# Optimization experiments

Measured on AMD Instinct MI355X. Metric: run time of the kernel, lower is better.

## Reference

```python
import jax, jax.numpy as jnp
import numpy as np

N = 8192
IN_F = 300
OUT_F = 300
ALPHA = 0.3  # leaky relu slope
NEG_INF = -1e12


def setup_inputs() -> dict:
    key = jax.random.key(0)
    k1, k2, k3, k4, k5 = jax.random.split(key, 5)
    inp = jax.random.normal(k1, (N, IN_F), dtype=jnp.float32)
    adj = jax.random.randint(k2, (N, N), 0, 2, dtype=jnp.int32)
    # xavier-uniform-like init for params
    def xavier(k, shape):
        fan_in, fan_out = shape[0], shape[1]
        limit = 1.414 * (6.0 / (fan_in + fan_out)) ** 0.5
        return jax.random.uniform(k, shape, jnp.float32, -limit, limit)
    W = xavier(k3, (IN_F, OUT_F))
    a = xavier(k4, (2 * OUT_F, 1))
    wtrans = xavier(k5, (2 * IN_F, OUT_F))
    return {"inp": inp, "adj": adj, "W": W, "a": a, "wtrans": wtrans}


def reference(inp, adj, W, a, wtrans):
    # h: [N, OUT_F]
    h = inp @ W
    Wh1 = h @ a[:OUT_F, :]          # [N, 1]
    Wh2 = h @ a[OUT_F:, :]          # [N, 1]
    e = jax.nn.leaky_relu(Wh1 + Wh2.T, negative_slope=ALPHA)  # [N, N]
    mask = adj > 0
    attention = jax.nn.softmax(jnp.where(mask, e, NEG_INF), axis=1)
    negative_attention = -jax.nn.softmax(jnp.where(mask, -e, NEG_INF), axis=1)
    # dropout p=0.0 / eval mode -> identity
    h_prime = attention @ inp                 # [N, IN_F]
    h_prime_negative = negative_attention @ inp
    h_prime_double = jnp.concatenate([h_prime, h_prime_negative], axis=1)  # [N, 2*IN_F]
    new_h_prime = h_prime_double @ wtrans     # [N, OUT_F]
    return jax.nn.elu(new_h_prime)  # concat=True
```

## Files before the change

kernel.cpp:

```cpp
#include <hip/hip_runtime.h>
#include <stdint.h>

#define NROW 8192
#define LOG2E 1.4426950408889634f
#define ALPHA 0.3f

#define WA1_OFF 0
#define WA2_OFF 512
#define S1_OFF 1024
#define S2_OFF (1024 + 8192)
#define SCAL_OFF (S2_OFF + 8192)
#define PQB_OFF 70656
#define PQB_BYTES (256 * 40960)
#define AMSK_OFF (PQB_OFF + PQB_BYTES)
#define AMSK_BYTES (NROW * 256 * 4)
#define PART_OFF (AMSK_OFF + AMSK_BYTES)

typedef _Float16 f16x8 __attribute__((ext_vector_type(8)));
typedef __fp16 fp16x2 __attribute__((ext_vector_type(2)));
typedef float f32x4 __attribute__((ext_vector_type(4)));

union HPack { fp16x2 h2[4]; f16x8 v; uint32_t u[4]; };
union HBits { _Float16 h[2]; uint32_t u; };

__device__ __forceinline__ int swz(int col, int g) { return (g + (col >> 1)) & 3; }

__global__ void k_wa(const float* __restrict__ Wm, const float* __restrict__ a,
                     float* __restrict__ wsf) {
  int r = blockIdx.x * 4 + (threadIdx.x >> 6);
  int ln = threadIdx.x & 63;
  if (r >= 300) return;
  float a1 = 0.f, a2 = 0.f;
  for (int c = ln; c < 300; c += 64) {
    float w = Wm[r * 300 + c];
    a1 += w * a[c];
    a2 += w * a[300 + c];
  }
  for (int o = 32; o; o >>= 1) { a1 += __shfl_down(a1, o); a2 += __shfl_down(a2, o); }
  if (!ln) { wsf[WA1_OFF + r] = a1; wsf[WA2_OFF + r] = a2; }
}

__global__ void k_s12(const float* __restrict__ inp, float* __restrict__ wsf) {
  int row = blockIdx.x * 4 + (threadIdx.x >> 6);
  int ln = threadIdx.x & 63;
  const float* ip = inp + (size_t)row * 300;
  float a1 = 0.f, a2 = 0.f;
  for (int c = ln; c < 300; c += 64) {
    float v = ip[c];
    a1 += v * wsf[WA1_OFF + c];
    a2 += v * wsf[WA2_OFF + c];
  }
  for (int o = 32; o; o >>= 1) { a1 += __shfl_down(a1, o); a2 += __shfl_down(a2, o); }
  if (!ln) { wsf[S1_OFF + row] = a1 * LOG2E; wsf[S2_OFF + row] = a2 * LOG2E; }
}

__global__ void k_minmax(float* __restrict__ wsf) {
  int t = threadIdx.x;
  float mx = -3e38f, mn = 3e38f;
  for (int i = t; i < NROW; i += 1024) {
    float v = wsf[S2_OFF + i];
    mx = fmaxf(mx, v); mn = fminf(mn, v);
  }
  for (int o = 32; o; o >>= 1) {
    mx = fmaxf(mx, __shfl_down(mx, o));
    mn = fminf(mn, __shfl_down(mn, o));
  }
  __shared__ float sm[32];
  int wv = t >> 6, ln = t & 63;
  if (!ln) { sm[wv] = mx; sm[16 + wv] = mn; }
  __syncthreads();
  if (!t) {
    float M = sm[0], m = sm[16];
    for (int q = 1; q < 16; q++) { M = fmaxf(M, sm[q]); m = fminf(m, sm[16 + q]); }
    wsf[SCAL_OFF] = M; wsf[SCAL_OFF + 1] = m;
  }
}

__global__ __launch_bounds__(256) void k_pack(const int* __restrict__ adj,
                                              uint32_t* __restrict__ amask) {
  const size_t t = (size_t)blockIdx.x * 256 + threadIdx.x;
  const int4* src = (const int4*)(adj + t * 32);
  uint32_t m = 0;
  #pragma unroll
  for (int j = 0; j < 8; j++) {
    int4 v = src[j];
    m |= (v.x ? 1u : 0u) << (4 * j);
    m |= (v.y ? 1u : 0u) << (4 * j + 1);
    m |= (v.z ? 1u : 0u) << (4 * j + 2);
    m |= (v.w ? 1u : 0u) << (4 * j + 3);
  }
  amask[t] = m;
}

__global__ __launch_bounds__(640) void k_wt(const float* __restrict__ inp,
                                            const float* __restrict__ wt,
                                            uint16_t* __restrict__ pqb) {
  __shared__ float L[300 * 36];
  const int kb = blockIdx.x;
  const int t = threadIdx.x;
  const float* src = inp + (size_t)kb * 32 * 300;
  for (int idx = t; idx < 9600; idx += 640) {
    int j = idx / 300;
    int c = idx - j * 300;
    L[c * 36 + j] = src[idx];
  }
  __syncthreads();
  if (t < 608) {
    const int pq = (t >= 304) ? 1 : 0;
    const int f = t - pq * 304;
    float acc[32];
    if (f < 300) {
      #pragma unroll
      for (int q = 0; q < 32; q++) acc[q] = 0.f;
      const float* wcol = wt + (size_t)pq * 90000 + f;
      for (int c = 0; c < 300; c++) {
        float wv = wcol[(size_t)c * 300];
        const float4* lp = (const float4*)(L + c * 36);
        #pragma unroll
        for (int q = 0; q < 8; q++) {
          float4 v = lp[q];
          acc[q * 4 + 0] += v.x * wv;
          acc[q * 4 + 1] += v.y * wv;
          acc[q * 4 + 2] += v.z * wv;
          acc[q * 4 + 3] += v.w * wv;
        }
      }
    } else {
      float cv = (f == 300) ? 1.0f : 0.0f;
      #pragma unroll
      for (int q = 0; q < 32; q++) acc[q] = cv;
    }
    uint16_t* dst = pqb + (size_t)kb * 20480 + (size_t)pq * 10240 + (size_t)f * 32;
    #pragma unroll
    for (int g = 0; g < 4; g++) {
      const int gs = swz(f, g);
      uint32_t* d32 = (uint32_t*)(dst + gs * 8);
      #pragma unroll
      for (int i = 0; i < 4; i++) {
        HBits hb;
        hb.h[0] = (_Float16)acc[g * 8 + 2 * i];
        hb.h[1] = (_Float16)acc[g * 8 + 2 * i + 1];
        d32[i] = hb.u;
      }
    }
  }
}

__global__ __launch_bounds__(512, 2) void k_main(const uint32_t* __restrict__ amask,
                                                 const float* __restrict__ wsf,
                                                 const uint16_t* __restrict__ pqb,
                                                 float* __restrict__ part, int nsplit) {
  __shared__ __align__(16) uint16_t Bsm[3][20480];
  const int bid = blockIdx.x;
  const int mblk = bid / nsplit;
  const int ks = bid - mblk * nsplit;
  const int tid = threadIdx.x;
  const int w = tid >> 6, lane = tid & 63;
  const int lr = lane & 15, lg = lane >> 4;
  const int side = w & 1;
  const int rg = w >> 1;
  const int rbase = mblk * 128 + rg * 32;
  const int row0 = rbase + lr;
  const int row1 = rbase + 16 + lr;
  const float c1_0 = wsf[S1_OFF + row0];
  const float c1_1 = wsf[S1_OFF + row1];
  const float s2ref = side ? wsf[SCAL_OFF + 1] : wsf[SCAL_OFF];
  const float sgn = side ? -1.0f : 1.0f;
  float tt0 = c1_0 + s2ref; const float so0 = sgn * fmaxf(tt0, ALPHA * tt0);
  float tt1 = c1_1 + s2ref; const float so1 = sgn * fmaxf(tt1, ALPHA * tt1);
  const int kcnt = NROW / nsplit;
  const int k0 = ks * kcnt;
  const int ksteps = kcnt >> 5;
  const int tb0 = k0 >> 5;
  const uint32_t* mr0 = amask + (size_t)row0 * 256;
  const uint32_t* mr1 = amask + (size_t)row1 * 256;
  f32x4 acc0[19], acc1[19];
  const f32x4 zero = {0.f, 0.f, 0.f, 0.f};
  #pragma unroll
  for (int ct = 0; ct < 19; ct++) { acc0[ct] = zero; acc1[ct] = zero; }

  auto STAGE = [&](int b, int tb) {
    const char* tile = (const char*)(pqb + (size_t)tb * 20480);
    char* dst = (char*)Bsm[b];
    #pragma unroll
    for (int it = 0; it < 5; it++) {
      const int off = (w * 5 + it) * 1024;
      __builtin_amdgcn_global_load_lds(
          (const __attribute__((address_space(1))) void*)(tile + off + lane * 16),
          (__attribute__((address_space(3))) void*)(dst + off),
          16, 0, 0);
    }
  };

  STAGE(0, tb0);
  uint32_t cM0 = mr0[tb0];
  uint32_t cM1 = mr1[tb0];
  const int kw0 = k0 + lg * 8;
  float4 cS0 = *(const float4*)(wsf + S2_OFF + kw0);
  float4 cS1 = *(const float4*)(wsf + S2_OFF + kw0 + 4);
  STAGE(1, (ksteps > 1) ? tb0 + 1 : tb0);

  for (int s = 0; s < ksteps; s++) {
    const int cur = s % 3;
    const int sp = (s + 1 < ksteps) ? s + 1 : s;
    const uint32_t nM0 = mr0[tb0 + sp];
    const uint32_t nM1 = mr1[tb0 + sp];
    const int kwn = k0 + sp * 32 + lg * 8;
    const float4 nS0 = *(const float4*)(wsf + S2_OFF + kwn);
    const float4 nS1 = *(const float4*)(wsf + S2_OFF + kwn + 4);

    asm volatile("s_waitcnt vmcnt(9)" ::: "memory");
    __builtin_amdgcn_sched_barrier(0);
    __builtin_amdgcn_s_barrier();

    const int st = (s + 2 < ksteps) ? s + 2 : ksteps - 1;
    STAGE((s + 2) % 3, tb0 + st);

    float se[8] = {cS0.x, cS0.y, cS0.z, cS0.w, cS1.x, cS1.y, cS1.z, cS1.w};
    const uint32_t b0 = (cM0 >> (lg * 8)) & 0xffu;
    const uint32_t b1 = (cM1 >> (lg * 8)) & 0xffu;
    HPack up0, up1;
    #pragma unroll
    for (int e = 0; e < 8; e += 2) {
      float e0a = c1_0 + se[e];     e0a = fmaxf(e0a, ALPHA * e0a);
      float e0b = c1_0 + se[e + 1]; e0b = fmaxf(e0b, ALPHA * e0b);
      float e1a = c1_1 + se[e];     e1a = fmaxf(e1a, ALPHA * e1a);
      float e1b = c1_1 + se[e + 1]; e1b = fmaxf(e1b, ALPHA * e1b);
      float p0a = exp2f(__builtin_fmaf(sgn, e0a, -so0)); p0a = (b0 & (1u << e)) ? p0a : 0.0f;
      float p0b = exp2f(__builtin_fmaf(sgn, e0b, -so0)); p0b = (b0 & (2u << e)) ? p0b : 0.0f;
      float p1a = exp2f(__builtin_fmaf(sgn, e1a, -so1)); p1a = (b1 & (1u << e)) ? p1a : 0.0f;
      float p1b = exp2f(__builtin_fmaf(sgn, e1b, -so1)); p1b = (b1 & (2u << e)) ? p1b : 0.0f;
      up0.h2[e >> 1] = __builtin_amdgcn_cvt_pkrtz(p0a, p0b);
      up1.h2[e >> 1] = __builtin_amdgcn_cvt_pkrtz(p1a, p1b);
    }

    const char* half = (const char*)Bsm[cur] + side * 20480;
    #pragma unroll
    for (int ct = 0; ct < 19; ct++) {
      const int col = ct * 16 + lr;
      const int gp = swz(col, lg);
      f16x8 b = *(const f16x8*)(half + col * 64 + gp * 16);
      acc0[ct] = __builtin_amdgcn_mfma_f32_16x16x32_f16(up0.v, b, acc0[ct], 0, 0, 0);
      acc1[ct] = __builtin_amdgcn_mfma_f32_16x16x32_f16(up1.v, b, acc1[ct], 0, 0, 0);
    }

    cM0 = nM0; cM1 = nM1; cS0 = nS0; cS1 = nS1;
  }

  float* pb = part + ((size_t)ks * NROW + rbase) * 608 + (size_t)side * 304;
  #pragma unroll
  for (int ct = 0; ct < 19; ct++) {
    const int col = ct * 16 + lr;
    #pragma unroll
    for (int r = 0; r < 4; r++) {
      pb[(size_t)(lg * 4 + r) * 608 + col] = acc0[ct][r];
      pb[(size_t)(16 + lg * 4 + r) * 608 + col] = acc1[ct][r];
    }
  }
}

__global__ void k_final(const float* __restrict__ part, float* __restrict__ out, int nsplit) {
  const int i = blockIdx.x;
  const int t = threadIdx.x;
  if (t >= 300) return;
  float sp = 0.f, sn = 0.f, zp = 0.f, zn = 0.f;
  for (int s = 0; s < nsplit; s++) {
    const float* p = part + ((size_t)s * NROW + i) * 608;
    sp += p[t];
    sn += p[304 + t];
    zp += p[300];
    zn += p[604];
  }
  float x = sp / zp - sn / zn;
  out[(size_t)i * 300 + t] = (x > 0.f) ? x : (exp2f(x * LOG2E) - 1.0f);
}

extern "C" void kernel_launch(void* const* d_in, const int* in_sizes, int n_in,
                              void* d_out, int out_size, void* d_ws, size_t ws_size,
                              hipStream_t stream) {
  const float* inp = (const float*)d_in[0];
  const int* adj = (const int*)d_in[1];
  const float* Wm = (const float*)d_in[2];
  const float* a = (const float*)d_in[3];
  const float* wt = (const float*)d_in[4];
  float* out = (float*)d_out;
  float* wsf = (float*)d_ws;
  uint16_t* pqb = (uint16_t*)((char*)d_ws + PQB_OFF);
  uint32_t* amask = (uint32_t*)((char*)d_ws + AMSK_OFF);
  float* part = (float*)((char*)d_ws + PART_OFF);

  int nsplit = 4;
  while (nsplit > 1 &&
         (size_t)PART_OFF + (size_t)nsplit * NROW * 608 * 4 > ws_size)
    nsplit >>= 1;

  k_wa<<<75, 256, 0, stream>>>(Wm, a, wsf);
  k_s12<<<NROW / 4, 256, 0, stream>>>(inp, wsf);
  k_minmax<<<1, 1024, 0, stream>>>(wsf);
  k_pack<<<NROW * NROW / 32 / 256, 256, 0, stream>>>(adj, amask);
  k_wt<<<256, 640, 0, stream>>>(inp, wt, pqb);
  k_main<<<64 * nsplit, 512, 0, stream>>>(amask, wsf, pqb, part, nsplit);
  k_final<<<NROW, 320, 0, stream>>>(part, out, nsplit);
}
```

Measured before the change: 270.6 us.

## Compute inp·wtrans with MFMA and fuse it with adjacency bit-packing

The fp32 scalar inp·wtrans projection is replaced by an fp16 MFMA GEMM. Wtrans is pre-converted to a swizzled fp16 layout by a new small kernel and streamed into LDS via double-buffered global_load_lds. The adjacency mask packing runs as extra blocks of the same launch, so the bandwidth-bound pack can overlap the compute-bound projection. s_setprio is also raised around the MFMA loop in k_main. The fp16 rounding of inp and wtrans before accumulation adds some precision loss.

```diff
diff --git a/kernel.cpp b/kernel.cpp
--- a/kernel.cpp
+++ b/kernel.cpp
@@ -14,14 +14,16 @@
 #define PQB_BYTES (256 * 40960)
 #define AMSK_OFF (PQB_OFF + PQB_BYTES)
 #define AMSK_BYTES (NROW * 256 * 4)
-#define PART_OFF (AMSK_OFF + AMSK_BYTES)
+#define WTF_OFF (AMSK_OFF + AMSK_BYTES)
+#define WTF_BYTES (10 * 40960)
+#define PART_OFF (WTF_OFF + WTF_BYTES)
 
 typedef _Float16 f16x8 __attribute__((ext_vector_type(8)));
 typedef __fp16 fp16x2 __attribute__((ext_vector_type(2)));
 typedef float f32x4 __attribute__((ext_vector_type(4)));
 
 union HPack { fp16x2 h2[4]; f16x8 v; uint32_t u[4]; };
-union HBits { _Float16 h[2]; uint32_t u; };
+union PkU { fp16x2 p; uint32_t u; };
 
 __device__ __forceinline__ int swz(int col, int g) { return (g + (col >> 1)) & 3; }
 
@@ -76,72 +78,129 @@
   }
 }
 
-__global__ __launch_bounds__(256) void k_pack(const int* __restrict__ adj,
-                                              uint32_t* __restrict__ amask) {
-  const size_t t = (size_t)blockIdx.x * 256 + threadIdx.x;
-  const int4* src = (const int4*)(adj + t * 32);
-  uint32_t m = 0;
-  #pragma unroll
-  for (int j = 0; j < 8; j++) {
-    int4 v = src[j];
-    m |= (v.x ? 1u : 0u) << (4 * j);
-    m |= (v.y ? 1u : 0u) << (4 * j + 1);
-    m |= (v.z ? 1u : 0u) << (4 * j + 2);
-    m |= (v.w ? 1u : 0u) << (4 * j + 3);
-  }
-  amask[t] = m;
-}
-
-__global__ __launch_bounds__(640) void k_wt(const float* __restrict__ inp,
-                                            const float* __restrict__ wt,
-                                            uint16_t* __restrict__ pqb) {
-  __shared__ float L[300 * 36];
-  const int kb = blockIdx.x;
-  const int t = threadIdx.x;
-  const float* src = inp + (size_t)kb * 32 * 300;
-  for (int idx = t; idx < 9600; idx += 640) {
-    int j = idx / 300;
-    int c = idx - j * 300;
-    L[c * 36 + j] = src[idx];
-  }
+__global__ __launch_bounds__(320) void k_wprep(const float* __restrict__ wt,
+                                               uint16_t* __restrict__ wtf) {
+  const int t = blockIdx.x >> 1;
+  const int pq = blockIdx.x & 1;
+  const int col = threadIdx.x;
+  uint16_t* dst = wtf + (size_t)t * 20480 + pq * 10240 + col * 32;
+  #pragma unroll
+  for (int g = 0; g < 4; g++) {
+    const int gs = swz(col, g);
+    uint32_t* d32 = (uint32_t*)(dst + gs * 8);
+    #pragma unroll
+    for (int jj = 0; jj < 4; jj++) {
+      const int c0 = t * 32 + g * 8 + 2 * jj;
+      float v0 = (col < 300 && c0 < 300) ? wt[(size_t)(pq * 300 + c0) * 300 + col] : 0.f;
+      float v1 = (col < 300 && c0 + 1 < 300) ? wt[(size_t)(pq * 300 + c0 + 1) * 300 + col] : 0.f;
+      PkU pk; pk.p = __builtin_amdgcn_cvt_pkrtz(v0, v1);
+      d32[jj] = pk.u;
+    }
+  }
+}
+
+#define WT_BLOCKS 256
+__global__ __launch_bounds__(640) void k_packwt(const int* __restrict__ adj,
+                                                uint32_t* __restrict__ amask,
+                                                const float* __restrict__ inp,
+                                                const uint16_t* __restrict__ wtf,
+                                                uint16_t* __restrict__ pqb) {
+  __shared__ __align__(16) uint16_t W2[2][20480];
+  const int bid = blockIdx.x;
+  const int tid = threadIdx.x;
+  if (bid >= WT_BLOCKS) {
+    const size_t wd = (size_t)(bid - WT_BLOCKS) * 640 + tid;
+    if (wd < (size_t)NROW * 256) {
+      const int4* src = (const int4*)(adj + wd * 32);
+      uint32_t m = 0;
+      #pragma unroll
+      for (int j = 0; j < 8; j++) {
+        int4 v = src[j];
+        m |= (v.x ? 1u : 0u) << (4 * j);
+        m |= (v.y ? 1u : 0u) << (4 * j + 1);
+        m |= (v.z ? 1u : 0u) << (4 * j + 2);
+        m |= (v.w ? 1u : 0u) << (4 * j + 3);
+      }
+      amask[wd] = m;
+    }
+    return;
+  }
+  const int kb = bid;
+  const int w = tid >> 6, lane = tid & 63;
+  const int lr = lane & 15, lg = lane >> 4;
+  const int side = (w >= 5) ? 1 : 0;
+  const int w5 = w - side * 5;
+  f32x4 acc[2][4];
+  const f32x4 zero = {0.f, 0.f, 0.f, 0.f};
+  #pragma unroll
+  for (int fr = 0; fr < 2; fr++)
+    #pragma unroll
+    for (int i = 0; i < 4; i++) acc[fr][i] = zero;
+
+  auto STAGE = [&](int b, int t) {
+    const char* tile = (const char*)wtf + (size_t)t * 40960;
+    char* dst = (char*)W2[b];
+    #pragma unroll
+    for (int it = 0; it < 4; it++) {
+      const int off = (w * 4 + it) * 1024;
+      __builtin_amdgcn_global_load_lds(
+          (const __attribute__((address_space(1))) void*)(tile + off + lane * 16),
+          (__attribute__((address_space(3))) void*)(dst + off),
+          16, 0, 0);
+    }
+  };
+
+  const float* arow0 = inp + (size_t)(kb * 32 + lr) * 300;
+  const float* arow1 = inp + (size_t)(kb * 32 + 16 + lr) * 300;
+
+  STAGE(0, 0);
   __syncthreads();
-  if (t < 608) {
-    const int pq = (t >= 304) ? 1 : 0;
-    const int f = t - pq * 304;
-    float acc[32];
-    if (f < 300) {
-      #pragma unroll
-      for (int q = 0; q < 32; q++) acc[q] = 0.f;
-      const float* wcol = wt + (size_t)pq * 90000 + f;
-      for (int c = 0; c < 300; c++) {
-        float wv = wcol[(size_t)c * 300];
-        const float4* lp = (const float4*)(L + c * 36);
-        #pragma unroll
-        for (int q = 0; q < 8; q++) {
-          float4 v = lp[q];
-          acc[q * 4 + 0] += v.x * wv;
-          acc[q * 4 + 1] += v.y * wv;
-          acc[q * 4 + 2] += v.z * wv;
-          acc[q * 4 + 3] += v.w * wv;
-        }
+  for (int t = 0; t < 10; t++) {
+    if (t < 9) STAGE((t + 1) & 1, t + 1);
+    const int c = t * 32 + lg * 8;
+    float4 z4 = {0.f, 0.f, 0.f, 0.f};
+    float4 a0l = z4, a0h = z4, a1l = z4, a1h = z4;
+    if (c <= 296) { a0l = *(const float4*)(arow0 + c); a1l = *(const float4*)(arow1 + c); }
+    if (c <= 292) { a0h = *(const float4*)(arow0 + c + 4); a1h = *(const float4*)(arow1 + c + 4); }
+    HPack A0, A1;
+    A0.h2[0] = __builtin_amdgcn_cvt_pkrtz(a0l.x, a0l.y);
+    A0.h2[1] = __builtin_amdgcn_cvt_pkrtz(a0l.z, a0l.w);
+    A0.h2[2] = __builtin_amdgcn_cvt_pkrtz(a0h.x, a0h.y);
+    A0.h2[3] = __builtin_amdgcn_cvt_pkrtz(a0h.z, a0h.w);
+    A1.h2[0] = __builtin_amdgcn_cvt_pkrtz(a1l.x, a1l.y);
+    A1.h2[1] = __builtin_amdgcn_cvt_pkrtz(a1l.z, a1l.w);
+    A1.h2[2] = __builtin_amdgcn_cvt_pkrtz(a1h.x, a1h.y);
+    A1.h2[3] = __builtin_amdgcn_cvt_pkrtz(a1h.z, a1h.w);
+    const char* half = (const char*)W2[t & 1] + side * 20480;
+    #pragma unroll
+    for (int i = 0; i < 4; i++) {
+      const int f = w5 * 4 + i;
+      if (f < 19) {
+        const int col = f * 16 + lr;
+        f16x8 b = *(const f16x8*)(half + col * 64 + swz(col, lg) * 16);
+        acc[0][i] = __builtin_amdgcn_mfma_f32_16x16x32_f16(A0.v, b, acc[0][i], 0, 0, 0);
+        acc[1][i] = __builtin_amdgcn_mfma_f32_16x16x32_f16(A1.v, b, acc[1][i], 0, 0, 0);
       }
-    } else {
-      float cv = (f == 300) ? 1.0f : 0.0f;
-      #pragma unroll
-      for (int q = 0; q < 32; q++) acc[q] = cv;
-    }
-    uint16_t* dst = pqb + (size_t)kb * 20480 + (size_t)pq * 10240 + (size_t)f * 32;
-    #pragma unroll
-    for (int g = 0; g < 4; g++) {
-      const int gs = swz(f, g);
-      uint32_t* d32 = (uint32_t*)(dst + gs * 8);
-      #pragma unroll
-      for (int i = 0; i < 4; i++) {
-        HBits hb;
-        hb.h[0] = (_Float16)acc[g * 8 + 2 * i];
-        hb.h[1] = (_Float16)acc[g * 8 + 2 * i + 1];
-        d32[i] = hb.u;
-      }
+    }
+    __syncthreads();
+  }
+  uint16_t* outb = pqb + (size_t)kb * 20480 + side * 10240;
+  #pragma unroll
+  for (int i = 0; i < 4; i++) {
+    const int f = w5 * 4 + i;
+    if (f >= 19) continue;
+    const int col = f * 16 + lr;
+    #pragma unroll
+    for (int fr = 0; fr < 2; fr++) {
+      float v0 = acc[fr][i][0], v1 = acc[fr][i][1], v2 = acc[fr][i][2], v3 = acc[fr][i][3];
+      if (col == 300) { v0 = v1 = v2 = v3 = 1.0f; }
+      else if (col > 300) { v0 = v1 = v2 = v3 = 0.0f; }
+      const int g = fr * 2 + (lg >> 1);
+      uint32_t* dst = (uint32_t*)(outb + col * 32 + swz(col, g) * 8 + (lg & 1) * 4);
+      PkU p0; p0.p = __builtin_amdgcn_cvt_pkrtz(v0, v1);
+      PkU p1; p1.p = __builtin_amdgcn_cvt_pkrtz(v2, v3);
+      dst[0] = p0.u;
+      dst[1] = p1.u;
     }
   }
 }
@@ -235,6 +294,7 @@
     }
 
     const char* half = (const char*)Bsm[cur] + side * 20480;
+    __builtin_amdgcn_s_setprio(1);
     #pragma unroll
     for (int ct = 0; ct < 19; ct++) {
       const int col = ct * 16 + lr;
@@ -243,6 +303,7 @@
       acc0[ct] = __builtin_amdgcn_mfma_f32_16x16x32_f16(up0.v, b, acc0[ct], 0, 0, 0);
       acc1[ct] = __builtin_amdgcn_mfma_f32_16x16x32_f16(up1.v, b, acc1[ct], 0, 0, 0);
     }
+    __builtin_amdgcn_s_setprio(0);
 
     cM0 = nM0; cM1 = nM1; cS0 = nS0; cS1 = nS1;
   }
@@ -287,6 +348,7 @@
   float* wsf = (float*)d_ws;
   uint16_t* pqb = (uint16_t*)((char*)d_ws + PQB_OFF);
   uint32_t* amask = (uint32_t*)((char*)d_ws + AMSK_OFF);
+  uint16_t* wtf = (uint16_t*)((char*)d_ws + WTF_OFF);
   float* part = (float*)((char*)d_ws + PART_OFF);
 
   int nsplit = 4;
@@ -294,11 +356,12 @@
          (size_t)PART_OFF + (size_t)nsplit * NROW * 608 * 4 > ws_size)
     nsplit >>= 1;
 
+  const int pack_blocks = (NROW * 256 + 639) / 640;
   k_wa<<<75, 256, 0, stream>>>(Wm, a, wsf);
+  k_wprep<<<20, 320, 0, stream>>>(wt, wtf);
   k_s12<<<NROW / 4, 256, 0, stream>>>(inp, wsf);
   k_minmax<<<1, 1024, 0, stream>>>(wsf);
-  k_pack<<<NROW * NROW / 32 / 256, 256, 0, stream>>>(adj, amask);
-  k_wt<<<256, 640, 0, stream>>>(inp, wt, pqb);
+  k_packwt<<<WT_BLOCKS + pack_blocks, 640, 0, stream>>>(adj, amask, inp, wtf, pqb);
   k_main<<<64 * nsplit, 512, 0, stream>>>(amask, wsf, pqb, part, nsplit);
   k_final<<<NROW, 320, 0, stream>>>(part, out, nsplit);
 }
```

Result: faster. 252.6 us (-6.7%).
